# Kernel tuning notes

Measured on AMD Instinct MI355X. Metric: run time of the kernel, lower is better.

The kernel has to match this reference:

```python
import jax, jax.numpy as jnp
import numpy as np

EPS = 1e-6
K = 20
NEG_SLOPE = 0.2

def knn_idx(x, k):
    # x: (B, D, N) flattened vector features; returns (B, N, k) neighbor indices
    inner = -2.0 * jnp.einsum('bdn,bdm->bnm', x, x)
    xx = jnp.sum(x * x, axis=1)  # (B, N)
    pd = -xx[:, :, None] - inner - xx[:, None, :]  # negative squared distance
    _, idx = jax.lax.top_k(pd, k)
    return idx

def get_graph_feature(x, k):
    # x: (B, C, 3, N) -> (B, 2C, 3, N, k) edge features (nbr - ctr, ctr)
    B, C, _, N = x.shape
    idx = knn_idx(x.reshape(B, C * 3, N), k)           # (B, N, k)
    feat = jnp.transpose(x, (0, 3, 1, 2))              # (B, N, C, 3)
    nb = jax.vmap(lambda f, i: f[i])(feat, idx)        # (B, N, k, C, 3)
    ctr = jnp.broadcast_to(feat[:, :, None], nb.shape)
    out = jnp.concatenate([nb - ctr, ctr], axis=3)     # (B, N, k, 2C, 3)
    return jnp.transpose(out, (0, 3, 4, 1, 2))

def vn_batchnorm(x, gamma, beta):
    # x: (B, C, 3, ...); BatchNorm (training stats) applied to vector norms
    norm = jnp.linalg.norm(x, axis=2) + EPS            # (B, C, ...)
    axes = (0,) + tuple(range(2, norm.ndim))
    mu = jnp.mean(norm, axis=axes, keepdims=True)
    var = jnp.var(norm, axis=axes, keepdims=True)
    shape = (1, -1) + (1,) * (norm.ndim - 2)
    nbn = (norm - mu) / jnp.sqrt(var + 1e-5) * gamma.reshape(shape) + beta.reshape(shape)
    return x / norm[:, :, None] * nbn[:, :, None]

def vn_linear_leakyrelu(x, w_feat, w_dir, gamma, beta):
    # x: (B, Cin, 3, ...) -> (B, Cout, 3, ...)
    p = jnp.einsum('oc,bc...->bo...', w_feat, x)
    p = vn_batchnorm(p, gamma, beta)
    d = jnp.einsum('oc,bc...->bo...', w_dir, x)
    dot = jnp.sum(p * d, axis=2, keepdims=True)
    dsq = jnp.sum(d * d, axis=2, keepdims=True)
    proj = p - (dot / (dsq + EPS)) * d
    return NEG_SLOPE * p + (1.0 - NEG_SLOPE) * jnp.where(dot >= 0, p, proj)

def _forward(x, w1, d1, g1, b1, w2, d2, g2, b2, w3, d3, g3, b3, w4, d4, g4, b4, w5, d5, g5, b5):
    h = jnp.transpose(x, (0, 2, 1))[:, None]           # (B, 1, 3, N)
    h = vn_linear_leakyrelu(get_graph_feature(h, K), w1, d1, g1, b1)
    x1 = jnp.mean(h, axis=-1)                          # mean_pool over k: (B, 21, 3, N)
    h = vn_linear_leakyrelu(get_graph_feature(x1, K), w2, d2, g2, b2)
    x2 = jnp.mean(h, axis=-1)                          # (B, 21, 3, N)
    h = vn_linear_leakyrelu(get_graph_feature(x2, K), w3, d3, g3, b3)
    x3 = jnp.mean(h, axis=-1)                          # (B, 42, 3, N)
    h = vn_linear_leakyrelu(get_graph_feature(x3, K), w4, d4, g4, b4)
    x4 = jnp.mean(h, axis=-1)                          # (B, 85, 3, N)
    cat = jnp.concatenate([x1, x2, x3, x4], axis=1)    # (B, 169, 3, N)
    return vn_linear_leakyrelu(cat, w5, d5, g5, b5)    # (B, 341, 3, N)

def setup_inputs():
    key = jax.random.key(0)
    B, N = 8, 1024
    d = {"x": jax.random.normal(key, (B, N, 3), dtype=jnp.float32)}
    feat_shapes = {"1": (21, 2), "2": (21, 42), "3": (42, 42), "4": (85, 84), "5": (341, 169)}
    dir_out = {"1": 21, "2": 21, "3": 42, "4": 85, "5": 1}  # conv5 shares nonlinearity -> 1 dir channel
    for i, (name, (co, ci)) in enumerate(feat_shapes.items()):
        k1, k2 = jax.random.split(jax.random.fold_in(key, i + 1))
        s = 1.0 / np.sqrt(ci)
        d["w" + name] = jax.random.uniform(k1, (co, ci), minval=-s, maxval=s, dtype=jnp.float32)
        d["d" + name] = jax.random.uniform(k2, (dir_out[name], ci), minval=-s, maxval=s, dtype=jnp.float32)
        d["g" + name] = jnp.ones((co,), dtype=jnp.float32)
        d["b" + name] = jnp.zeros((co,), dtype=jnp.float32)
    return d

def reference(x, w1, d1, g1, b1, w2, d2, g2, b2, w3, d3, g3, b3, w4, d4, g4, b4, w5, d5, g5, b5):
    return _forward(x, w1, d1, g1, b1, w2, d2, g2, b2, w3, d3, g3, b3, w4, d4, g4, b4, w5, d5, g5, b5)
```

## Files before the change

kernel.cpp:

```cpp
#include <hip/hip_runtime.h>
#include <math.h>

#define KNN 20
#define NS 0.2f
#define EPSV 1e-6f
#define QT 4
#define OT 8
#define TN 8
#define CROW 507
#define SSPLIT 8

struct F3 { float x, y, z; };

extern __shared__ __align__(16) float smem[];

__global__ void k_transpose(const float* __restrict__ x, float* __restrict__ xt,
                            float* __restrict__ xx, int B, int N) {
    int i = blockIdx.x * blockDim.x + threadIdx.x;
    if (i >= B * N) return;
    int b = i / N, n = i % N;
    const float* src = x + (size_t)(b * N + n) * 3;
    float* dst = xt + (size_t)b * 3 * N + n;
    float s0 = src[0], s1 = src[1], s2 = src[2];
    dst[0] = s0;
    dst[(size_t)N] = s1;
    dst[(size_t)2 * N] = s2;
    float s = 0.f;
    s += s0 * s0;
    s += s1 * s1;
    s += s2 * s2;
    xx[i] = s;
}

__global__ void k_knn(const float* __restrict__ X, const float* __restrict__ xx,
                      int* __restrict__ idx,
                      int N, int D, long batchStride, long sliceOff) {
    int b = blockIdx.y;
    int q0 = blockIdx.x * QT;
    int tid = threadIdx.x;
    int lane = tid & 63;
    int wave = tid >> 6;

    __shared__ __align__(16) float qf[128 * QT];
    __shared__ __align__(16) float pd[QT][1024];

    const float* Xb = X + (size_t)b * batchStride + sliceOff;
    const float* xxb = xx + (size_t)b * N;

    for (int t = tid; t < QT * D; t += 256) {
        int d = t >> 2, q = t & 3;
        qf[d * QT + q] = Xb[(size_t)d * N + (q0 + q)];
    }
    __syncthreads();

    float a0x = 0.f, a0y = 0.f, a0z = 0.f, a0w = 0.f;
    float a1x = 0.f, a1y = 0.f, a1z = 0.f, a1w = 0.f;
    float a2x = 0.f, a2y = 0.f, a2z = 0.f, a2w = 0.f;
    float a3x = 0.f, a3y = 0.f, a3z = 0.f, a3w = 0.f;

    const float* mbase = Xb + 4 * tid;
#pragma unroll 3
    for (int d = 0; d < D; ++d) {
        float4 xm = *(const float4*)(mbase + (size_t)d * N);
        float4 qv = *(const float4*)(qf + d * QT);
        a0x += qv.x * xm.x; a0y += qv.x * xm.y; a0z += qv.x * xm.z; a0w += qv.x * xm.w;
        a1x += qv.y * xm.x; a1y += qv.y * xm.y; a1z += qv.y * xm.z; a1w += qv.y * xm.w;
        a2x += qv.z * xm.x; a2y += qv.z * xm.y; a2z += qv.z * xm.z; a2w += qv.z * xm.w;
        a3x += qv.w * xm.x; a3y += qv.w * xm.y; a3z += qv.w * xm.z; a3w += qv.w * xm.w;
    }

    {
        float4 m2 = *(const float4*)(xxb + 4 * tid);
        float4 qn = *(const float4*)(xxb + q0);
        float4 v;
        v.x = 2.f * a0x - qn.x - m2.x; v.y = 2.f * a0y - qn.x - m2.y;
        v.z = 2.f * a0z - qn.x - m2.z; v.w = 2.f * a0w - qn.x - m2.w;
        *(float4*)&pd[0][4 * tid] = v;
        v.x = 2.f * a1x - qn.y - m2.x; v.y = 2.f * a1y - qn.y - m2.y;
        v.z = 2.f * a1z - qn.y - m2.z; v.w = 2.f * a1w - qn.y - m2.w;
        *(float4*)&pd[1][4 * tid] = v;
        v.x = 2.f * a2x - qn.z - m2.x; v.y = 2.f * a2y - qn.z - m2.y;
        v.z = 2.f * a2z - qn.z - m2.z; v.w = 2.f * a2w - qn.z - m2.w;
        *(float4*)&pd[2][4 * tid] = v;
        v.x = 2.f * a3x - qn.w - m2.x; v.y = 2.f * a3y - qn.w - m2.y;
        v.z = 2.f * a3z - qn.w - m2.z; v.w = 2.f * a3w - qn.w - m2.w;
        *(float4*)&pd[3][4 * tid] = v;
    }
    __syncthreads();

    unsigned long long key[16];
#pragma unroll
    for (int t = 0; t < 16; ++t) {
        unsigned u = __float_as_uint(pd[wave][t * 64 + lane]);
        u ^= (unsigned)((int)u >> 31) | 0x80000000u;
        unsigned lo = (unsigned)(1023 - t * 64) - (unsigned)lane;
        key[t] = ((unsigned long long)u << 32) | (unsigned long long)lo;
    }

#define CE(a, b)                                        \
    {                                                   \
        unsigned long long ka = key[a], kb = key[b];    \
        bool sw = ka < kb;                              \
        key[a] = sw ? kb : ka;                          \
        key[b] = sw ? ka : kb;                          \
    }
    CE(0,1) CE(2,3) CE(4,5) CE(6,7) CE(8,9) CE(10,11) CE(12,13) CE(14,15)
    CE(0,2) CE(1,3) CE(4,6) CE(5,7) CE(8,10) CE(9,11) CE(12,14) CE(13,15)
    CE(1,2) CE(5,6) CE(9,10) CE(13,14)
    CE(0,4) CE(1,5) CE(2,6) CE(3,7) CE(8,12) CE(9,13) CE(10,14) CE(11,15)
    CE(2,4) CE(3,5) CE(10,12) CE(11,13)
    CE(1,2) CE(3,4) CE(5,6) CE(9,10) CE(11,12) CE(13,14)
    CE(0,8) CE(1,9) CE(2,10) CE(3,11) CE(4,12) CE(5,13) CE(6,14) CE(7,15)
    CE(4,8) CE(5,9) CE(6,10) CE(7,11)
    CE(2,4) CE(3,5) CE(6,8) CE(7,9) CE(10,12) CE(11,13)
    CE(1,2) CE(3,4) CE(5,6) CE(7,8) CE(9,10) CE(11,12) CE(13,14)
#undef CE

    __syncthreads();
    unsigned long long* kl = (unsigned long long*)&pd[wave][0];
#pragma unroll
    for (int t = 8; t < 16; ++t) kl[(t - 8) * 64 + lane] = key[t];
    int nspill = 0;

    long outBase = ((long)b * N + q0 + wave) * KNN;
    for (int it = 0; it < KNN; ++it) {
        unsigned myh = (unsigned)(key[0] >> 32);
        unsigned mylo = (unsigned)(key[0] & 0xFFFFFFFFull);
        unsigned bh = myh;
#pragma unroll
        for (int off = 32; off >= 1; off >>= 1) {
            unsigned oh = __shfl_xor(bh, off, 64);
            if (oh > bh) bh = oh;
        }
        unsigned long long mask = __ballot(myh == bh);
        unsigned ml;
        if (__popcll(mask) == 1) {
            int src = (int)(__ffsll((long long)mask) - 1);
            ml = __shfl(mylo, src, 64);
        } else {
            unsigned cand = (myh == bh) ? mylo : 0u;
#pragma unroll
            for (int off = 32; off >= 1; off >>= 1) {
                unsigned oc = __shfl_xor(cand, off, 64);
                if (oc > cand) cand = oc;
            }
            ml = cand;
        }
        int bi = 1023 - (int)(ml & 1023u);
        if (lane == 0) idx[outBase + it] = bi;
        if ((bi & 63) == lane) {
            key[0] = key[1]; key[1] = key[2]; key[2] = key[3]; key[3] = key[4];
            key[4] = key[5]; key[5] = key[6]; key[6] = key[7];
            int sidx = nspill < 8 ? nspill : 7;
            unsigned long long nv = kl[sidx * 64 + lane];
            key[7] = (nspill < 8) ? nv : 0ull;
            nspill++;
        }
    }
}

__global__ void k_matmul_pair_lds(const float* __restrict__ X, const float* __restrict__ W,
                                  const float* __restrict__ Dw,
                                  float* __restrict__ U, float* __restrict__ V,
                                  float* __restrict__ UD, float* __restrict__ VD,
                                  int C, int Co, int CoP, int TILE,
                                  int rowStride, int colOff) {
    const int CP = C * CoP;
    float* wts = smem;
    float* xs = smem + 4 * CP;

    int tid = threadIdx.x;
    int bn0 = blockIdx.x * TILE;
    int C3 = C * 3;

    int npad = CoP - Co;
    if (npad) {
        for (int t = tid; t < 4 * C * npad; t += 256) {
            int q = t / npad, oo = Co + t % npad;
            int mat = q / C, c = q % C;
            wts[mat * CP + c * CoP + oo] = 0.f;
        }
    }
    int twoCC = 2 * C * Co;
    for (int t = tid; t < twoCC; t += 256) {
        int o = t / (2 * C), c = t % (2 * C);
        float w = W[t], dw = Dw[t];
        if (c < C) {
            wts[c * CoP + o] = w;
            wts[2 * CP + c * CoP + o] = dw;
        } else {
            wts[CP + (c - C) * CoP + o] = w;
            wts[3 * CP + (c - C) * CoP + o] = dw;
        }
    }
    for (int t = tid; t < TILE * C3; t += 256) {
        int p = t / C3, cc = t % C3;
        xs[t] = X[(size_t)(bn0 + p) * rowStride + colOff + cc];
    }
    __syncthreads();
    for (int t = tid; t < CP; t += 256) {
        wts[CP + t] -= wts[t];
        wts[3 * CP + t] -= wts[2 * CP + t];
    }
    __syncthreads();

    int GPP = CoP >> 2;
    int items = TILE * GPP;
    for (int e = tid; e < items; e += 256) {
        int p = e / GPP, og = e - p * GPP;
        int o0 = og * 4;
        const float* xr = xs + p * C3;

        float aU[4][3], aV[4][3], aDu[4][3], aDv[4][3];
#pragma unroll
        for (int i = 0; i < 4; ++i)
#pragma unroll
            for (int j = 0; j < 3; ++j) {
                aU[i][j] = 0.f; aV[i][j] = 0.f; aDu[i][j] = 0.f; aDv[i][j] = 0.f;
            }

        for (int c = 0; c < C; ++c) {
            float x0 = xr[c * 3], x1 = xr[c * 3 + 1], x2 = xr[c * 3 + 2];
            const float* wp = wts + c * CoP + o0;
            float4 wa4 = *(const float4*)(wp);
            float4 wb4 = *(const float4*)(wp + CP);
            float4 da4 = *(const float4*)(wp + 2 * CP);
            float4 db4 = *(const float4*)(wp + 3 * CP);
            float wav[4] = {wa4.x, wa4.y, wa4.z, wa4.w};
            float wbv[4] = {wb4.x, wb4.y, wb4.z, wb4.w};
            float dav[4] = {da4.x, da4.y, da4.z, da4.w};
            float dbv[4] = {db4.x, db4.y, db4.z, db4.w};
#pragma unroll
            for (int i = 0; i < 4; ++i) {
                aU[i][0] += wav[i] * x0; aU[i][1] += wav[i] * x1; aU[i][2] += wav[i] * x2;
                aV[i][0] += wbv[i] * x0; aV[i][1] += wbv[i] * x1; aV[i][2] += wbv[i] * x2;
                aDu[i][0] += dav[i] * x0; aDu[i][1] += dav[i] * x1; aDu[i][2] += dav[i] * x2;
                aDv[i][0] += dbv[i] * x0; aDv[i][1] += dbv[i] * x1; aDv[i][2] += dbv[i] * x2;
            }
        }

        size_t base = ((size_t)(bn0 + p) * Co + o0) * 3;
#pragma unroll
        for (int i = 0; i < 4; ++i) {
            int o = o0 + i;
            if (o < Co) {
                size_t off = base + (size_t)i * 3;
                U[off] = aU[i][0]; U[off + 1] = aU[i][1]; U[off + 2] = aU[i][2];
                V[off] = aV[i][0]; V[off + 1] = aV[i][1]; V[off + 2] = aV[i][2];
                UD[off] = aDu[i][0]; UD[off + 1] = aDu[i][1]; UD[off + 2] = aDu[i][2];
                VD[off] = aDv[i][0]; VD[off + 1] = aDv[i][1]; VD[off + 2] = aDv[i][2];
            }
        }
    }
}

__global__ void k_stats_edge_det(const float* __restrict__ U, const float* __restrict__ V,
                                 const int* __restrict__ idx, float* __restrict__ partials,
                                 int N, int Co, int BN) {
    int o = blockIdx.x;
    int s = blockIdx.y;
    int tid = threadIdx.x;
    int P = BN / SSPLIT;
    int g0 = s * P;

    __shared__ float Ush[3072];
    __shared__ float r1[256], r2[256];

    for (int t = tid; t < P; t += 256) {
        F3 u3 = *(const F3*)(U + ((size_t)(g0 + t) * Co + o) * 3);
        Ush[t * 3 + 0] = u3.x;
        Ush[t * 3 + 1] = u3.y;
        Ush[t * 3 + 2] = u3.z;
    }
    __syncthreads();

    float s1 = 0.f, s2 = 0.f;
    for (int pl = tid; pl < P; pl += 256) {
        int g = g0 + pl;
        F3 v3 = *(const F3*)(V + ((size_t)g * Co + o) * 3);
        float v0 = v3.x, v1 = v3.y, v2 = v3.z;
        const int* ip = idx + (size_t)g * KNN;
        for (int kk = 0; kk < KNN; ++kk) {
            const float* Ur = Ush + ip[kk] * 3;
            float p0 = Ur[0] + v0;
            float p1 = Ur[1] + v1;
            float p2 = Ur[2] + v2;
            float nm = sqrtf(p0 * p0 + p1 * p1 + p2 * p2) + EPSV;
            s1 += nm;
            s2 += nm * nm;
        }
    }
    r1[tid] = s1; r2[tid] = s2;
    __syncthreads();
    for (int st = 128; st > 0; st >>= 1) {
        if (tid < st) { r1[tid] += r1[tid + st]; r2[tid] += r2[tid + st]; }
        __syncthreads();
    }
    if (tid == 0) {
        partials[(o * SSPLIT + s) * 2] = r1[0];
        partials[(o * SSPLIT + s) * 2 + 1] = r2[0];
    }
}

__global__ void k_final_fused(const float* __restrict__ U, const float* __restrict__ V,
                              const float* __restrict__ UD, const float* __restrict__ VD,
                              const int* __restrict__ idx, const float* __restrict__ partials,
                              const float* __restrict__ gamma, const float* __restrict__ beta,
                              float* __restrict__ catp, float* __restrict__ catn,
                              float* __restrict__ xx,
                              int N, int Co, int colOff, float cnt, int doSq) {
    int b = blockIdx.y;
    int n0 = blockIdx.x * TN;
    int tid = threadIdx.x;
    int CC = Co * 3;

    __shared__ float tile[TN * 255];
    __shared__ float muS[85], invS[85];

    for (int o = tid; o < Co; o += 256) {
        float s1 = 0.f, s2 = 0.f;
        for (int s = 0; s < SSPLIT; ++s) {
            s1 += partials[(o * SSPLIT + s) * 2];
            s2 += partials[(o * SSPLIT + s) * 2 + 1];
        }
        float mu = s1 / cnt;
        float var = s2 / cnt - mu * mu;
        muS[o] = mu;
        invS[o] = rsqrtf(var + 1e-5f);
    }
    __syncthreads();

    const float invk = 1.f / (float)KNN;
    int items = TN * Co;
    for (int e = tid; e < items; e += 256) {
        int nl = e / Co, o = e - nl * Co;
        int n = n0 + nl;
        float mu = muS[o], inv = invS[o];
        float gmm = gamma[o], bt = beta[o];

        size_t ctr = ((size_t)(b * N + n) * Co + o) * 3;
        F3 vc = *(const F3*)(V + ctr);
        F3 wc = *(const F3*)(VD + ctr);
        float v0 = vc.x, v1 = vc.y, v2 = vc.z;
        float w0 = wc.x, w1 = wc.y, w2 = wc.z;
        const int* ip = idx + ((size_t)b * N + n) * KNN;

        float a0 = 0.f, a1 = 0.f, a2 = 0.f;
        for (int kk = 0; kk < KNN; ++kk) {
            int m = ip[kk];
            size_t nb = ((size_t)(b * N + m) * Co + o) * 3;
            F3 un = *(const F3*)(U + nb);
            F3 dn = *(const F3*)(UD + nb);
            float p0 = un.x + v0;
            float p1 = un.y + v1;
            float p2 = un.z + v2;
            float nm = sqrtf(p0 * p0 + p1 * p1 + p2 * p2) + EPSV;
            float nbn = (nm - mu) * inv * gmm + bt;
            float sc = nbn / nm;
            p0 *= sc; p1 *= sc; p2 *= sc;
            float d0 = dn.x + w0;
            float d1 = dn.y + w1;
            float d2 = dn.z + w2;
            float dot = p0 * d0 + p1 * d1 + p2 * d2;
            if (dot >= 0.f) {
                a0 += p0; a1 += p1; a2 += p2;
            } else {
                float f = dot / (d0 * d0 + d1 * d1 + d2 * d2 + EPSV);
                a0 += NS * p0 + (1.f - NS) * (p0 - f * d0);
                a1 += NS * p1 + (1.f - NS) * (p1 - f * d1);
                a2 += NS * p2 + (1.f - NS) * (p2 - f * d2);
            }
        }
        tile[nl * CC + o * 3 + 0] = a0 * invk;
        tile[nl * CC + o * 3 + 1] = a1 * invk;
        tile[nl * CC + o * 3 + 2] = a2 * invk;
    }
    __syncthreads();

    for (int t = tid; t < TN * CC; t += 256) {
        int nl = t / CC, c = t - nl * CC;
        catp[(size_t)(b * N + n0 + nl) * CROW + colOff + c] = tile[nl * CC + c];
    }
    for (int t = tid; t < TN * CC; t += 256) {
        int c = t >> 3, nl = t & (TN - 1);
        catn[(size_t)b * CROW * N + (size_t)(colOff + c) * N + n0 + nl] = tile[nl * CC + c];
    }
    if (doSq && tid < TN) {
        const float* row = tile + tid * CC;
        float s = 0.f;
        for (int c = 0; c < CC; ++c) {
            float v = row[c];
            s += v * v;
        }
        xx[(size_t)b * N + n0 + tid] = s;
    }
}

__global__ void k_matmul_plain(const float* __restrict__ X, const float* __restrict__ W,
                               const float* __restrict__ Dw,
                               float* __restrict__ U, float* __restrict__ Ud,
                               int N, int Cin, int Cout, long batchStride, long sliceOff) {
    int ot = blockIdx.y;
    int b = blockIdx.z;
    int tid = threadIdx.x;
    int n = blockIdx.x * 512 + 2 * tid;

    const float* Wp; float* Up; int CoutE; int o0;
    if (ot == (int)gridDim.y - 1) {
        Wp = Dw; Up = Ud; CoutE = 1; o0 = 0;
    } else {
        Wp = W; Up = U; CoutE = Cout; o0 = ot * OT;
    }

    __shared__ __align__(16) float wsm[OT][176];
    for (int t = tid; t < OT * Cin; t += 256) {
        int oo = t / Cin, c = t % Cin;
        int o = o0 + oo;
        wsm[oo][c] = (o < CoutE) ? Wp[(size_t)o * Cin + c] : 0.f;
    }
    __syncthreads();

    const float* Xp = X + (size_t)b * batchStride + sliceOff + n;
    float au[OT][3][2];
#pragma unroll
    for (int oo = 0; oo < OT; ++oo)
#pragma unroll
        for (int j = 0; j < 3; ++j) {
            au[oo][j][0] = 0.f; au[oo][j][1] = 0.f;
        }

    int c = 0;
    for (; c + 4 <= Cin; c += 4) {
        float2 xv[4][3];
#pragma unroll
        for (int cc = 0; cc < 4; ++cc)
#pragma unroll
            for (int j = 0; j < 3; ++j)
                xv[cc][j] = *(const float2*)(Xp + ((size_t)(c + cc) * 3 + j) * N);
#pragma unroll
        for (int oo = 0; oo < OT; ++oo) {
            float4 w4 = *(const float4*)&wsm[oo][c];
            float wv[4] = {w4.x, w4.y, w4.z, w4.w};
#pragma unroll
            for (int j = 0; j < 3; ++j) {
#pragma unroll
                for (int cc = 0; cc < 4; ++cc) {
                    au[oo][j][0] += wv[cc] * xv[cc][j].x;
                    au[oo][j][1] += wv[cc] * xv[cc][j].y;
                }
            }
        }
    }
    for (; c < Cin; ++c) {
        float2 xv[3];
#pragma unroll
        for (int j = 0; j < 3; ++j)
            xv[j] = *(const float2*)(Xp + ((size_t)c * 3 + j) * N);
#pragma unroll
        for (int oo = 0; oo < OT; ++oo) {
            float wv = wsm[oo][c];
#pragma unroll
            for (int j = 0; j < 3; ++j) {
                au[oo][j][0] += wv * xv[j].x;
                au[oo][j][1] += wv * xv[j].y;
            }
        }
    }
#pragma unroll
    for (int oo = 0; oo < OT; ++oo) {
        int o = o0 + oo;
        if (o < CoutE) {
#pragma unroll
            for (int j = 0; j < 3; ++j) {
                float2 st; st.x = au[oo][j][0]; st.y = au[oo][j][1];
                *(float2*)&Up[(((size_t)b * CoutE + o) * 3 + j) * N + n] = st;
            }
        }
    }
}

__global__ void k_stats_plain_det(const float* __restrict__ U, float* __restrict__ mv,
                                  int N, int Cout, int BN, float cnt) {
    int o = blockIdx.x;
    int tid = threadIdx.x;
    float s1 = 0.f, s2 = 0.f;
    for (int g = tid; g < BN; g += 256) {
        int b = g / N, n = g % N;
        const float* Ub = U + (((size_t)b * Cout + o) * 3) * N;
        float p0 = Ub[n], p1 = Ub[(size_t)N + n], p2 = Ub[(size_t)2 * N + n];
        float nm = sqrtf(p0 * p0 + p1 * p1 + p2 * p2) + EPSV;
        s1 += nm;
        s2 += nm * nm;
    }
    __shared__ float r1[256], r2[256];
    r1[tid] = s1; r2[tid] = s2;
    __syncthreads();
    for (int st = 128; st > 0; st >>= 1) {
        if (tid < st) { r1[tid] += r1[tid + st]; r2[tid] += r2[tid + st]; }
        __syncthreads();
    }
    if (tid == 0) {
        float mu = r1[0] / cnt;
        float var = r2[0] / cnt - mu * mu;
        mv[2 * o] = mu;
        mv[2 * o + 1] = rsqrtf(var + 1e-5f);
    }
}

__global__ void k_final_plain(const float* __restrict__ U, const float* __restrict__ Dv,
                              const float* __restrict__ mv,
                              const float* __restrict__ gamma, const float* __restrict__ beta,
                              float* __restrict__ out, int N, int Cout) {
    int b = blockIdx.z, o = blockIdx.y, tid = threadIdx.x;
    int n = blockIdx.x * 256 + tid;
    float mu = mv[2 * o];
    float inv = mv[2 * o + 1];
    float g = gamma[o], bt = beta[o];

    const float* Ub = U + (((size_t)b * Cout + o) * 3) * N;
    float p0 = Ub[n], p1 = Ub[(size_t)N + n], p2 = Ub[(size_t)2 * N + n];
    float nm = sqrtf(p0 * p0 + p1 * p1 + p2 * p2) + EPSV;
    float nbn = (nm - mu) * inv * g + bt;
    float sc = nbn / nm;
    p0 *= sc; p1 *= sc; p2 *= sc;

    float d0 = Dv[((size_t)b * 3 + 0) * N + n];
    float d1 = Dv[((size_t)b * 3 + 1) * N + n];
    float d2 = Dv[((size_t)b * 3 + 2) * N + n];
    float dot = p0 * d0 + p1 * d1 + p2 * d2;
    float o0, o1, o2;
    if (dot >= 0.f) {
        o0 = p0; o1 = p1; o2 = p2;
    } else {
        float f = dot / (d0 * d0 + d1 * d1 + d2 * d2 + EPSV);
        o0 = NS * p0 + (1.f - NS) * (p0 - f * d0);
        o1 = NS * p1 + (1.f - NS) * (p1 - f * d1);
        o2 = NS * p2 + (1.f - NS) * (p2 - f * d2);
    }
    size_t ob = (((size_t)b * Cout + o) * 3) * N + n;
    out[ob] = o0;
    out[ob + (size_t)N] = o1;
    out[ob + (size_t)2 * N] = o2;
}

extern "C" void kernel_launch(void* const* d_in, const int* in_sizes, int n_in,
                              void* d_out, int out_size, void* d_ws, size_t ws_size,
                              hipStream_t stream) {
    (void)in_sizes; (void)n_in; (void)out_size; (void)ws_size;
    const int B = 8, N = 1024;

    const float* x = (const float*)d_in[0];
    const float* W[5]; const float* Dw[5]; const float* G[5]; const float* Bt[5];
    for (int l = 0; l < 5; ++l) {
        W[l]  = (const float*)d_in[1 + 4 * l];
        Dw[l] = (const float*)d_in[2 + 4 * l];
        G[l]  = (const float*)d_in[3 + 4 * l];
        Bt[l] = (const float*)d_in[4 + 4 * l];
    }

    float* ws = (float*)d_ws;
    size_t off = 0;
    float* xt = ws + off;     off += (size_t)B * 3 * N;
    int* idx = (int*)(ws + off); off += (size_t)B * N * KNN;
    float* catp = ws + off;   off += (size_t)B * N * CROW;
    float* catn = ws + off;   off += (size_t)B * N * CROW;
    float* Up = ws + off;     off += (size_t)B * N * 85 * 3;
    float* Vp = ws + off;     off += (size_t)B * N * 85 * 3;
    float* UDp = ws + off;    off += (size_t)B * N * 85 * 3;
    float* VDp = ws + off;    off += (size_t)B * N * 85 * 3;
    float* U5 = ws + off;     off += (size_t)B * 341 * 3 * N;
    float* d5buf = ws + off;  off += (size_t)B * 3 * N;
    float* xx = ws + off;     off += (size_t)B * N;
    float* partials = ws + off; off += (size_t)341 * SSPLIT * 2;
    float* mv = ws + off;     off += 2 * 341;

    k_transpose<<<(B * N + 255) / 256, 256, 0, stream>>>(x, xt, xx, B, N);

    const int Cin_[4]  = {1, 21, 21, 42};
    const int Cout_[4] = {21, 21, 42, 85};
    const int inOff_[4] = {-1, 0, 21, 42};
    const int outOff_[4] = {0, 21, 42, 84};
    const int Tile_[4] = {32, 32, 32, 8};

    const int BN = B * N;

    for (int l = 0; l < 4; ++l) {
        int C = Cin_[l], Co = Cout_[l];
        int D = C * 3;
        int CoP = (Co + 3) & ~3;
        int TILE = Tile_[l];

        const float* Xn; long bs, so;
        if (inOff_[l] < 0) { Xn = xt; bs = (long)3 * N; so = 0; }
        else { Xn = catn; bs = (long)CROW * N; so = (long)inOff_[l] * 3 * N; }

        const float* Xp; int rs, co;
        if (inOff_[l] < 0) { Xp = x; rs = 3; co = 0; }
        else { Xp = catp; rs = CROW; co = inOff_[l] * 3; }

        dim3 gk(N / QT, B);
        k_knn<<<gk, 256, 0, stream>>>(Xn, xx, idx, N, D, bs, so);

        size_t smemB = (size_t)(4 * C * CoP + TILE * C * 3) * sizeof(float);
        k_matmul_pair_lds<<<(B * N) / TILE, 256, smemB, stream>>>(
            Xp, W[l], Dw[l], Up, Vp, UDp, VDp, C, Co, CoP, TILE, rs, co);

        dim3 gst(Co, SSPLIT);
        k_stats_edge_det<<<gst, 256, 0, stream>>>(Up, Vp, idx, partials, N, Co, BN);

        int doSq = (l < 3) ? 1 : 0;
        dim3 gf(N / TN, B);
        k_final_fused<<<gf, 256, 0, stream>>>(
            Up, Vp, UDp, VDp, idx, partials, G[l], Bt[l],
            catp, catn, xx, N, Co, outOff_[l] * 3,
            (float)((size_t)BN * KNN), doSq);
    }

    {
        long bs = (long)CROW * N, so = 0;
        dim3 gm5(N / 512, (341 + OT - 1) / OT + 1, B);
        k_matmul_plain<<<gm5, 256, 0, stream>>>(catn, W[4], Dw[4], U5, d5buf,
                                                N, 169, 341, bs, so);
        k_stats_plain_det<<<341, 256, 0, stream>>>(U5, mv, N, 341, BN, (float)BN);
        dim3 gs5(N / 256, 341, B);
        k_final_plain<<<gs5, 256, 0, stream>>>(U5, d5buf, mv, G[4], Bt[4],
                                               (float*)d_out, N, 341);
    }
}
```

Measured before the change: 664.5 us.

## Fuse kNN and edge-matmul into one launch with block-role split

Merges the kNN kernel and the per-point pair matmul into one kernel. The first mmBlocks blocks run the matmul and the remaining blocks run kNN, so the two independent stages can overlap across CUs without a launch boundary between them. For layers 1-3 each kNN block now handles 8 queries in a loop over 4-query chunks, and layer 3's matmul tile shrinks from 32 to 16. Layer 4 still uses separate launches. The shared dynamic LDS allocation is sized to the larger of the two needs, which may lower occupancy for the matmul blocks.

```diff
diff --git a/kernel.cpp b/kernel.cpp
--- a/kernel.cpp
+++ b/kernel.cpp
@@ -32,130 +32,233 @@
     xx[i] = s;
 }
 
-__global__ void k_knn(const float* __restrict__ X, const float* __restrict__ xx,
-                      int* __restrict__ idx,
-                      int N, int D, long batchStride, long sliceOff) {
-    int b = blockIdx.y;
-    int q0 = blockIdx.x * QT;
+__global__ void k_knn_mm(
+                         const float* __restrict__ Xn, const float* __restrict__ xx,
+                         int* __restrict__ idx, int N, int D,
+                         long batchStride, long sliceOff, int qPerBlock,
+                         const float* __restrict__ Xp, const float* __restrict__ W,
+                         const float* __restrict__ Dw,
+                         float* __restrict__ U, float* __restrict__ V,
+                         float* __restrict__ UD, float* __restrict__ VD,
+                         int C, int Co, int CoP, int TILE,
+                         int rowStride, int colOff, int mmBlocks) {
+    float* sm = smem;
     int tid = threadIdx.x;
+
+    if ((int)blockIdx.x < mmBlocks) {
+        const int CP = C * CoP;
+        float* wts = sm;
+        float* xs = sm + 4 * CP;
+        int bn0 = blockIdx.x * TILE;
+        int C3 = C * 3;
+
+        int npad = CoP - Co;
+        if (npad) {
+            for (int t = tid; t < 4 * C * npad; t += 256) {
+                int q = t / npad, oo = Co + t % npad;
+                int mat = q / C, c = q % C;
+                wts[mat * CP + c * CoP + oo] = 0.f;
+            }
+        }
+        int twoCC = 2 * C * Co;
+        for (int t = tid; t < twoCC; t += 256) {
+            int o = t / (2 * C), c = t % (2 * C);
+            float w = W[t], dw = Dw[t];
+            if (c < C) {
+                wts[c * CoP + o] = w;
+                wts[2 * CP + c * CoP + o] = dw;
+            } else {
+                wts[CP + (c - C) * CoP + o] = w;
+                wts[3 * CP + (c - C) * CoP + o] = dw;
+            }
+        }
+        for (int t = tid; t < TILE * C3; t += 256) {
+            int p = t / C3, cc = t % C3;
+            xs[t] = Xp[(size_t)(bn0 + p) * rowStride + colOff + cc];
+        }
+        __syncthreads();
+        for (int t = tid; t < CP; t += 256) {
+            wts[CP + t] -= wts[t];
+            wts[3 * CP + t] -= wts[2 * CP + t];
+        }
+        __syncthreads();
+
+        int GPP = CoP >> 2;
+        int items = TILE * GPP;
+        for (int e = tid; e < items; e += 256) {
+            int p = e / GPP, og = e - p * GPP;
+            int o0 = og * 4;
+            const float* xr = xs + p * C3;
+
+            float aU[4][3], aV[4][3], aDu[4][3], aDv[4][3];
+#pragma unroll
+            for (int i = 0; i < 4; ++i)
+#pragma unroll
+                for (int j = 0; j < 3; ++j) {
+                    aU[i][j] = 0.f; aV[i][j] = 0.f; aDu[i][j] = 0.f; aDv[i][j] = 0.f;
+                }
+
+            for (int c = 0; c < C; ++c) {
+                float x0 = xr[c * 3], x1 = xr[c * 3 + 1], x2 = xr[c * 3 + 2];
+                const float* wp = wts + c * CoP + o0;
+                float4 wa4 = *(const float4*)(wp);
+                float4 wb4 = *(const float4*)(wp + CP);
+                float4 da4 = *(const float4*)(wp + 2 * CP);
+                float4 db4 = *(const float4*)(wp + 3 * CP);
+                float wav[4] = {wa4.x, wa4.y, wa4.z, wa4.w};
+                float wbv[4] = {wb4.x, wb4.y, wb4.z, wb4.w};
+                float dav[4] = {da4.x, da4.y, da4.z, da4.w};
+                float dbv[4] = {db4.x, db4.y, db4.z, db4.w};
+#pragma unroll
+                for (int i = 0; i < 4; ++i) {
+                    aU[i][0] += wav[i] * x0; aU[i][1] += wav[i] * x1; aU[i][2] += wav[i] * x2;
+                    aV[i][0] += wbv[i] * x0; aV[i][1] += wbv[i] * x1; aV[i][2] += wbv[i] * x2;
+                    aDu[i][0] += dav[i] * x0; aDu[i][1] += dav[i] * x1; aDu[i][2] += dav[i] * x2;
+                    aDv[i][0] += dbv[i] * x0; aDv[i][1] += dbv[i] * x1; aDv[i][2] += dbv[i] * x2;
+                }
+            }
+
+            size_t base = ((size_t)(bn0 + p) * Co + o0) * 3;
+#pragma unroll
+            for (int i = 0; i < 4; ++i) {
+                int o = o0 + i;
+                if (o < Co) {
+                    size_t off = base + (size_t)i * 3;
+                    U[off] = aU[i][0]; U[off + 1] = aU[i][1]; U[off + 2] = aU[i][2];
+                    V[off] = aV[i][0]; V[off + 1] = aV[i][1]; V[off + 2] = aV[i][2];
+                    UD[off] = aDu[i][0]; UD[off + 1] = aDu[i][1]; UD[off + 2] = aDu[i][2];
+                    VD[off] = aDv[i][0]; VD[off + 1] = aDv[i][1]; VD[off + 2] = aDv[i][2];
+                }
+            }
+        }
+        return;
+    }
+
+    int kb = (int)blockIdx.x - mmBlocks;
+    int qbpb = N / qPerBlock;
+    int b = kb / qbpb;
+    int qbase = (kb - b * qbpb) * qPerBlock;
     int lane = tid & 63;
     int wave = tid >> 6;
 
-    __shared__ __align__(16) float qf[128 * QT];
-    __shared__ __align__(16) float pd[QT][1024];
-
-    const float* Xb = X + (size_t)b * batchStride + sliceOff;
+    float* qf = sm;
+    float* pdb = sm + 128 * QT;
+
+    const float* Xb = Xn + (size_t)b * batchStride + sliceOff;
     const float* xxb = xx + (size_t)b * N;
 
-    for (int t = tid; t < QT * D; t += 256) {
-        int d = t >> 2, q = t & 3;
-        qf[d * QT + q] = Xb[(size_t)d * N + (q0 + q)];
-    }
-    __syncthreads();
-
-    float a0x = 0.f, a0y = 0.f, a0z = 0.f, a0w = 0.f;
-    float a1x = 0.f, a1y = 0.f, a1z = 0.f, a1w = 0.f;
-    float a2x = 0.f, a2y = 0.f, a2z = 0.f, a2w = 0.f;
-    float a3x = 0.f, a3y = 0.f, a3z = 0.f, a3w = 0.f;
-
-    const float* mbase = Xb + 4 * tid;
+    for (int q0 = qbase; q0 < qbase + qPerBlock; q0 += QT) {
+        for (int t = tid; t < QT * D; t += 256) {
+            int d = t >> 2, q = t & 3;
+            qf[d * QT + q] = Xb[(size_t)d * N + (q0 + q)];
+        }
+        __syncthreads();
+
+        float a0x = 0.f, a0y = 0.f, a0z = 0.f, a0w = 0.f;
+        float a1x = 0.f, a1y = 0.f, a1z = 0.f, a1w = 0.f;
+        float a2x = 0.f, a2y = 0.f, a2z = 0.f, a2w = 0.f;
+        float a3x = 0.f, a3y = 0.f, a3z = 0.f, a3w = 0.f;
+
+        const float* mbase = Xb + 4 * tid;
 #pragma unroll 3
-    for (int d = 0; d < D; ++d) {
-        float4 xm = *(const float4*)(mbase + (size_t)d * N);
-        float4 qv = *(const float4*)(qf + d * QT);
-        a0x += qv.x * xm.x; a0y += qv.x * xm.y; a0z += qv.x * xm.z; a0w += qv.x * xm.w;
-        a1x += qv.y * xm.x; a1y += qv.y * xm.y; a1z += qv.y * xm.z; a1w += qv.y * xm.w;
-        a2x += qv.z * xm.x; a2y += qv.z * xm.y; a2z += qv.z * xm.z; a2w += qv.z * xm.w;
-        a3x += qv.w * xm.x; a3y += qv.w * xm.y; a3z += qv.w * xm.z; a3w += qv.w * xm.w;
-    }
-
-    {
-        float4 m2 = *(const float4*)(xxb + 4 * tid);
-        float4 qn = *(const float4*)(xxb + q0);
-        float4 v;
-        v.x = 2.f * a0x - qn.x - m2.x; v.y = 2.f * a0y - qn.x - m2.y;
-        v.z = 2.f * a0z - qn.x - m2.z; v.w = 2.f * a0w - qn.x - m2.w;
-        *(float4*)&pd[0][4 * tid] = v;
-        v.x = 2.f * a1x - qn.y - m2.x; v.y = 2.f * a1y - qn.y - m2.y;
-        v.z = 2.f * a1z - qn.y - m2.z; v.w = 2.f * a1w - qn.y - m2.w;
-        *(float4*)&pd[1][4 * tid] = v;
-        v.x = 2.f * a2x - qn.z - m2.x; v.y = 2.f * a2y - qn.z - m2.y;
-        v.z = 2.f * a2z - qn.z - m2.z; v.w = 2.f * a2w - qn.z - m2.w;
-        *(float4*)&pd[2][4 * tid] = v;
-        v.x = 2.f * a3x - qn.w - m2.x; v.y = 2.f * a3y - qn.w - m2.y;
-        v.z = 2.f * a3z - qn.w - m2.z; v.w = 2.f * a3w - qn.w - m2.w;
-        *(float4*)&pd[3][4 * tid] = v;
-    }
-    __syncthreads();
-
-    unsigned long long key[16];
-#pragma unroll
-    for (int t = 0; t < 16; ++t) {
-        unsigned u = __float_as_uint(pd[wave][t * 64 + lane]);
-        u ^= (unsigned)((int)u >> 31) | 0x80000000u;
-        unsigned lo = (unsigned)(1023 - t * 64) - (unsigned)lane;
-        key[t] = ((unsigned long long)u << 32) | (unsigned long long)lo;
-    }
+        for (int d = 0; d < D; ++d) {
+            float4 xm = *(const float4*)(mbase + (size_t)d * N);
+            float4 qv = *(const float4*)(qf + d * QT);
+            a0x += qv.x * xm.x; a0y += qv.x * xm.y; a0z += qv.x * xm.z; a0w += qv.x * xm.w;
+            a1x += qv.y * xm.x; a1y += qv.y * xm.y; a1z += qv.y * xm.z; a1w += qv.y * xm.w;
+            a2x += qv.z * xm.x; a2y += qv.z * xm.y; a2z += qv.z * xm.z; a2w += qv.z * xm.w;
+            a3x += qv.w * xm.x; a3y += qv.w * xm.y; a3z += qv.w * xm.z; a3w += qv.w * xm.w;
+        }
+
+        {
+            float4 m2 = *(const float4*)(xxb + 4 * tid);
+            float4 qn = *(const float4*)(xxb + q0);
+            float4 v;
+            v.x = 2.f * a0x - qn.x - m2.x; v.y = 2.f * a0y - qn.x - m2.y;
+            v.z = 2.f * a0z - qn.x - m2.z; v.w = 2.f * a0w - qn.x - m2.w;
+            *(float4*)(pdb + 0 * 1024 + 4 * tid) = v;
+            v.x = 2.f * a1x - qn.y - m2.x; v.y = 2.f * a1y - qn.y - m2.y;
+            v.z = 2.f * a1z - qn.y - m2.z; v.w = 2.f * a1w - qn.y - m2.w;
+            *(float4*)(pdb + 1 * 1024 + 4 * tid) = v;
+            v.x = 2.f * a2x - qn.z - m2.x; v.y = 2.f * a2y - qn.z - m2.y;
+            v.z = 2.f * a2z - qn.z - m2.z; v.w = 2.f * a2w - qn.z - m2.w;
+            *(float4*)(pdb + 2 * 1024 + 4 * tid) = v;
+            v.x = 2.f * a3x - qn.w - m2.x; v.y = 2.f * a3y - qn.w - m2.y;
+            v.z = 2.f * a3z - qn.w - m2.z; v.w = 2.f * a3w - qn.w - m2.w;
+            *(float4*)(pdb + 3 * 1024 + 4 * tid) = v;
+        }
+        __syncthreads();
+
+        unsigned long long key[16];
+#pragma unroll
+        for (int t = 0; t < 16; ++t) {
+            unsigned u = __float_as_uint(pdb[wave * 1024 + t * 64 + lane]);
+            u ^= (unsigned)((int)u >> 31) | 0x80000000u;
+            unsigned lo = (unsigned)(1023 - t * 64) - (unsigned)lane;
+            key[t] = ((unsigned long long)u << 32) | (unsigned long long)lo;
+        }
 
 #define CE(a, b)                                        \
-    {                                                   \
-        unsigned long long ka = key[a], kb = key[b];    \
-        bool sw = ka < kb;                              \
-        key[a] = sw ? kb : ka;                          \
-        key[b] = sw ? ka : kb;                          \
-    }
-    CE(0,1) CE(2,3) CE(4,5) CE(6,7) CE(8,9) CE(10,11) CE(12,13) CE(14,15)
-    CE(0,2) CE(1,3) CE(4,6) CE(5,7) CE(8,10) CE(9,11) CE(12,14) CE(13,15)
-    CE(1,2) CE(5,6) CE(9,10) CE(13,14)
-    CE(0,4) CE(1,5) CE(2,6) CE(3,7) CE(8,12) CE(9,13) CE(10,14) CE(11,15)
-    CE(2,4) CE(3,5) CE(10,12) CE(11,13)
-    CE(1,2) CE(3,4) CE(5,6) CE(9,10) CE(11,12) CE(13,14)
-    CE(0,8) CE(1,9) CE(2,10) CE(3,11) CE(4,12) CE(5,13) CE(6,14) CE(7,15)
-    CE(4,8) CE(5,9) CE(6,10) CE(7,11)
-    CE(2,4) CE(3,5) CE(6,8) CE(7,9) CE(10,12) CE(11,13)
-    CE(1,2) CE(3,4) CE(5,6) CE(7,8) CE(9,10) CE(11,12) CE(13,14)
+        {                                               \
+            unsigned long long ka = key[a], kb2 = key[b]; \
+            bool sw = ka < kb2;                         \
+            key[a] = sw ? kb2 : ka;                     \
+            key[b] = sw ? ka : kb2;                     \
+        }
+        CE(0,1) CE(2,3) CE(4,5) CE(6,7) CE(8,9) CE(10,11) CE(12,13) CE(14,15)
+        CE(0,2) CE(1,3) CE(4,6) CE(5,7) CE(8,10) CE(9,11) CE(12,14) CE(13,15)
+        CE(1,2) CE(5,6) CE(9,10) CE(13,14)
+        CE(0,4) CE(1,5) CE(2,6) CE(3,7) CE(8,12) CE(9,13) CE(10,14) CE(11,15)
+        CE(2,4) CE(3,5) CE(10,12) CE(11,13)
+        CE(1,2) CE(3,4) CE(5,6) CE(9,10) CE(11,12) CE(13,14)
+        CE(0,8) CE(1,9) CE(2,10) CE(3,11) CE(4,12) CE(5,13) CE(6,14) CE(7,15)
+        CE(4,8) CE(5,9) CE(6,10) CE(7,11)
+        CE(2,4) CE(3,5) CE(6,8) CE(7,9) CE(10,12) CE(11,13)
+        CE(1,2) CE(3,4) CE(5,6) CE(7,8) CE(9,10) CE(11,12) CE(13,14)
 #undef CE
 
-    __syncthreads();
-    unsigned long long* kl = (unsigned long long*)&pd[wave][0];
-#pragma unroll
-    for (int t = 8; t < 16; ++t) kl[(t - 8) * 64 + lane] = key[t];
-    int nspill = 0;
-
-    long outBase = ((long)b * N + q0 + wave) * KNN;
-    for (int it = 0; it < KNN; ++it) {
-        unsigned myh = (unsigned)(key[0] >> 32);
-        unsigned mylo = (unsigned)(key[0] & 0xFFFFFFFFull);
-        unsigned bh = myh;
-#pragma unroll
-        for (int off = 32; off >= 1; off >>= 1) {
-            unsigned oh = __shfl_xor(bh, off, 64);
-            if (oh > bh) bh = oh;
-        }
-        unsigned long long mask = __ballot(myh == bh);
-        unsigned ml;
-        if (__popcll(mask) == 1) {
-            int src = (int)(__ffsll((long long)mask) - 1);
-            ml = __shfl(mylo, src, 64);
-        } else {
-            unsigned cand = (myh == bh) ? mylo : 0u;
+        __syncthreads();
+        unsigned long long* kl = (unsigned long long*)(pdb + wave * 1024);
+#pragma unroll
+        for (int t = 8; t < 16; ++t) kl[(t - 8) * 64 + lane] = key[t];
+        int nspill = 0;
+
+        long outBase = ((long)b * N + q0 + wave) * KNN;
+        for (int it = 0; it < KNN; ++it) {
+            unsigned myh = (unsigned)(key[0] >> 32);
+            unsigned mylo = (unsigned)(key[0] & 0xFFFFFFFFull);
+            unsigned bh = myh;
 #pragma unroll
             for (int off = 32; off >= 1; off >>= 1) {
-                unsigned oc = __shfl_xor(cand, off, 64);
-                if (oc > cand) cand = oc;
-            }
-            ml = cand;
-        }
-        int bi = 1023 - (int)(ml & 1023u);
-        if (lane == 0) idx[outBase + it] = bi;
-        if ((bi & 63) == lane) {
-            key[0] = key[1]; key[1] = key[2]; key[2] = key[3]; key[3] = key[4];
-            key[4] = key[5]; key[5] = key[6]; key[6] = key[7];
-            int sidx = nspill < 8 ? nspill : 7;
-            unsigned long long nv = kl[sidx * 64 + lane];
-            key[7] = (nspill < 8) ? nv : 0ull;
-            nspill++;
-        }
+                unsigned oh = __shfl_xor(bh, off, 64);
+                if (oh > bh) bh = oh;
+            }
+            unsigned long long mask = __ballot(myh == bh);
+            unsigned ml;
+            if (__popcll(mask) == 1) {
+                int src = (int)(__ffsll((long long)mask) - 1);
+                ml = __shfl(mylo, src, 64);
+            } else {
+                unsigned cand = (myh == bh) ? mylo : 0u;
+#pragma unroll
+                for (int off = 32; off >= 1; off >>= 1) {
+                    unsigned oc = __shfl_xor(cand, off, 64);
+                    if (oc > cand) cand = oc;
+                }
+                ml = cand;
+            }
+            int bi = 1023 - (int)(ml & 1023u);
+            if (lane == 0) idx[outBase + it] = bi;
+            if ((bi & 63) == lane) {
+                key[0] = key[1]; key[1] = key[2]; key[2] = key[3]; key[3] = key[4];
+                key[4] = key[5]; key[5] = key[6]; key[6] = key[7];
+                int sidx = nspill < 8 ? nspill : 7;
+                unsigned long long nv = kl[sidx * 64 + lane];
+                key[7] = (nspill < 8) ? nv : 0ull;
+                nspill++;
+            }
+        }
+        __syncthreads();
     }
 }
 
@@ -580,9 +683,10 @@
     const int Cout_[4] = {21, 21, 42, 85};
     const int inOff_[4] = {-1, 0, 21, 42};
     const int outOff_[4] = {0, 21, 42, 84};
-    const int Tile_[4] = {32, 32, 32, 8};
+    const int Tile_[4] = {32, 32, 16, 8};
 
     const int BN = B * N;
+    const size_t KNN_LDS = (size_t)(128 * QT + QT * 1024) * sizeof(float);
 
     for (int l = 0; l < 4; ++l) {
         int C = Cin_[l], Co = Cout_[l];
@@ -598,12 +702,22 @@
         if (inOff_[l] < 0) { Xp = x; rs = 3; co = 0; }
         else { Xp = catp; rs = CROW; co = inOff_[l] * 3; }
 
-        dim3 gk(N / QT, B);
-        k_knn<<<gk, 256, 0, stream>>>(Xn, xx, idx, N, D, bs, so);
-
-        size_t smemB = (size_t)(4 * C * CoP + TILE * C * 3) * sizeof(float);
-        k_matmul_pair_lds<<<(B * N) / TILE, 256, smemB, stream>>>(
-            Xp, W[l], Dw[l], Up, Vp, UDp, VDp, C, Co, CoP, TILE, rs, co);
+        size_t mmNeed = (size_t)(4 * C * CoP + TILE * C * 3) * sizeof(float);
+
+        if (l < 3) {
+            int mmB = BN / TILE;
+            int knnB = BN / 8;
+            size_t smemB = mmNeed > KNN_LDS ? mmNeed : KNN_LDS;
+            k_knn_mm<<<mmB + knnB, 256, smemB, stream>>>(
+                Xn, xx, idx, N, D, bs, so, 8,
+                Xp, W[l], Dw[l], Up, Vp, UDp, VDp, C, Co, CoP, TILE, rs, co, mmB);
+        } else {
+            k_knn_mm<<<BN / 4, 256, KNN_LDS, stream>>>(
+                Xn, xx, idx, N, D, bs, so, 4,
+                Xp, W[l], Dw[l], Up, Vp, UDp, VDp, C, Co, CoP, TILE, rs, co, 0);
+            k_matmul_pair_lds<<<BN / TILE, 256, mmNeed, stream>>>(
+                Xp, W[l], Dw[l], Up, Vp, UDp, VDp, C, Co, CoP, TILE, rs, co);
+        }
 
         dim3 gst(Co, SSPLIT);
         k_stats_edge_det<<<gst, 256, 0, stream>>>(Up, Vp, idx, partials, N, Co, BN);
```

Result: no change. 653.1 us (median of 2 runs) (-1.7%).
